# Kernel optimization log

Hardware: AMD Instinct MI355X
Metric: run time of the kernel (lower is better)

The kernel has to match this reference:

```python
import jax, jax.numpy as jnp
import numpy as np

H = 128          # hidden_channels
N_USER = 500000
N_ANIME = 20000
N_EDGE = 500000


def setup_inputs() -> dict:
    key = jax.random.key(0)
    k = jax.random.split(key, 8)
    s1 = 1.0 / np.sqrt(2 * H)   # torch Linear init scale (uniform bound)
    s2 = 1.0 / np.sqrt(H)
    return {
        "z_user": jax.random.normal(k[0], (N_USER, H), dtype=jnp.float32),
        "z_anime": jax.random.normal(k[1], (N_ANIME, H), dtype=jnp.float32),
        "row": jax.random.randint(k[2], (N_EDGE,), 0, N_USER, dtype=jnp.int64 if jax.config.jax_enable_x64 else jnp.int32),
        "col": jax.random.randint(k[3], (N_EDGE,), 0, N_ANIME, dtype=jnp.int64 if jax.config.jax_enable_x64 else jnp.int32),
        "W1": jax.random.uniform(k[4], (2 * H, H), minval=-s1, maxval=s1, dtype=jnp.float32),
        "b1": jnp.zeros((H,), dtype=jnp.float32),
        "W2": jax.random.uniform(k[5], (H, 1), minval=-s2, maxval=s2, dtype=jnp.float32),
        "b2": jnp.zeros((1,), dtype=jnp.float32),
    }


def reference(z_user, z_anime, row, col, W1, b1, W2, b2):
    zu = z_user[row]            # [E, H] gather
    za = z_anime[col]           # [E, H] gather
    # cat([zu, za], -1) @ W1 == zu @ W1[:H] + za @ W1[H:]  (avoids materializing concat)
    h = zu @ W1[:H] + za @ W1[H:] + b1          # [E, H]
    h = jax.nn.relu(h)
    out = h @ W2 + b2                            # [E, 1]
    return out.reshape(-1)
```

## Files before the change

kernel.cpp:

```cpp
#include <hip/hip_runtime.h>
#include <hip/hip_bf16.h>
#include <stdint.h>

#define H_ 128
#define THREADS 256
#define EPB 64

typedef __bf16 bf16x8 __attribute__((ext_vector_type(8)));
typedef float  f32x4  __attribute__((ext_vector_type(4)));


__device__ inline bf16x8 pack8(float4 a, float4 b) {
    bf16x8 v;
    v[0] = (__bf16)a.x; v[1] = (__bf16)a.y; v[2] = (__bf16)a.z; v[3] = (__bf16)a.w;
    v[4] = (__bf16)b.x; v[5] = (__bf16)b.y; v[6] = (__bf16)b.z; v[7] = (__bf16)b.w;
    return v;
}

__global__ void prep_kernel(const float* __restrict__ W1,
                            const float* __restrict__ za,
                            __bf16* __restrict__ wfrag,
                            __bf16* __restrict__ za_bf,
                            int nza) {
    int t = blockIdx.x * 256 + threadIdx.x;
    if (t < 32768) {
        int j  = t & 7;
        int ln = (t >> 3) & 63;
        int nt = (t >> 9) & 7;
        int ks = (t >> 12) & 7;
        int k  = ks * 32 + ((ln >> 4) << 3) + j;
        int n  = nt * 16 + (ln & 15);
        wfrag[t] = (__bf16)W1[k * H_ + n];
    } else {
        long i = (long)(t - 32768) * 8;
        if (i < nza) {
            float4 a = *(const float4*)(za + i);
            float4 b = *(const float4*)(za + i + 4);
            *(bf16x8*)(za_bf + i) = pack8(a, b);
        }
    }
}

__global__ __launch_bounds__(THREADS, 4)
void edge_decoder_kernel(const float* __restrict__ z_user,
                         const float* __restrict__ z_anime,
                         const int*   __restrict__ row,
                         const int*   __restrict__ col,
                         const float* __restrict__ W1,
                         const float* __restrict__ b1,
                         const float* __restrict__ W2,
                         const float* __restrict__ b2,
                         const __bf16* __restrict__ wfrag,
                         const __bf16* __restrict__ za_bf,
                         int use_ws,
                         float* __restrict__ out,
                         int E) {
    __shared__ bf16x8 Bf[4][8][64];

    const int tid  = threadIdx.x;
    const int lane = tid & 63;
    const int wv   = tid >> 6;
    const int g    = lane >> 4;
    const int m    = lane & 15;
    const int base = blockIdx.x * EPB + wv * 16;

    int e = base + m; if (e >= E) e = E - 1;
    const int r0 = row[e], c0 = col[e];

    float4 xu[8];
    {
        const float* zu = z_user + (size_t)r0 * H_ + g * 8;
        #pragma unroll
        for (int ks = 0; ks < 4; ++ks) {
            xu[2 * ks]     = *(const float4*)(zu + ks * 32);
            xu[2 * ks + 1] = *(const float4*)(zu + ks * 32 + 4);
        }
    }
    bf16x8 Aa[4];
    if (use_ws) {
        const __bf16* za = za_bf + (size_t)c0 * H_ + g * 8;
        #pragma unroll
        for (int ks = 0; ks < 4; ++ks)
            Aa[ks] = *(const bf16x8*)(za + ks * 32);
    }

    float w2v[8], b1v[8];
    #pragma unroll
    for (int nt = 0; nt < 8; ++nt) { int ch = nt * 16 + m; w2v[nt] = W2[ch]; b1v[nt] = b1[ch]; }
    const float bb = b2[0];

    if (use_ws) {
        const int4* src = (const int4*)wfrag;
        int4*       dst = (int4*)&Bf[0][0][0];
        #pragma unroll
        for (int i = 0; i < 8; ++i)
            dst[tid + i * THREADS] = src[tid + i * THREADS];
    } else {
        __bf16* d = (__bf16*)&Bf[0][0][0];
        for (int idx = tid; idx < H_ * H_; idx += THREADS) {
            int k = idx >> 7, n = idx & 127;
            int ks = k >> 5, gg = (k >> 3) & 3, j = k & 7;
            int nt = n >> 4, ln = (gg << 4) | (n & 15);
            d[ks * 4096 + nt * 512 + ln * 8 + j] = (__bf16)W1[k * H_ + n];
        }
    }
    __syncthreads();

    bf16x8 Au[4];
    #pragma unroll
    for (int ks = 0; ks < 4; ++ks)
        Au[ks] = pack8(xu[2 * ks], xu[2 * ks + 1]);

    f32x4 acc[8];
    #pragma unroll
    for (int nt = 0; nt < 8; ++nt) acc[nt] = (f32x4){0.f, 0.f, 0.f, 0.f};

    #pragma unroll
    for (int nt = 0; nt < 8; ++nt) {
        #pragma unroll
        for (int ks = 0; ks < 4; ++ks) {
            bf16x8 b = Bf[ks][nt][lane];
            acc[nt] = __builtin_amdgcn_mfma_f32_16x16x32_bf16(Au[ks], b, acc[nt], 0, 0, 0);
        }
    }

    if (!use_ws) {
        const float* za = z_anime + (size_t)c0 * H_ + g * 8;
        #pragma unroll
        for (int ks = 0; ks < 4; ++ks)
            Aa[ks] = pack8(*(const float4*)(za + ks * 32),
                           *(const float4*)(za + ks * 32 + 4));
    }

    __syncthreads();

    if (use_ws) {
        const int4* src = (const int4*)wfrag + 2048;
        int4*       dst = (int4*)&Bf[0][0][0];
        #pragma unroll
        for (int i = 0; i < 8; ++i)
            dst[tid + i * THREADS] = src[tid + i * THREADS];
    } else {
        __bf16* d = (__bf16*)&Bf[0][0][0];
        for (int idx = tid; idx < H_ * H_; idx += THREADS) {
            int k = idx >> 7, n = idx & 127;
            int ks = k >> 5, gg = (k >> 3) & 3, j = k & 7;
            int nt = n >> 4, ln = (gg << 4) | (n & 15);
            d[ks * 4096 + nt * 512 + ln * 8 + j] = (__bf16)W1[(H_ + k) * H_ + n];
        }
    }
    __syncthreads();

    #pragma unroll
    for (int nt = 0; nt < 8; ++nt) {
        #pragma unroll
        for (int ks = 0; ks < 4; ++ks) {
            bf16x8 b = Bf[ks][nt][lane];
            acc[nt] = __builtin_amdgcn_mfma_f32_16x16x32_bf16(Aa[ks], b, acc[nt], 0, 0, 0);
        }
    }

    float ps[4];
    #pragma unroll
    for (int r = 0; r < 4; ++r) {
        float s = 0.f;
        #pragma unroll
        for (int nt = 0; nt < 8; ++nt) {
            float h = acc[nt][r] + b1v[nt];
            s = fmaf(fmaxf(h, 0.f), w2v[nt], s);
        }
        ps[r] = s;
    }
    #pragma unroll
    for (int off = 1; off < 16; off <<= 1) {
        #pragma unroll
        for (int r = 0; r < 4; ++r)
            ps[r] += __shfl_xor(ps[r], off, 64);
    }
    if (m == 0) {
        int eb = base + g * 4;
        if (eb + 3 < E) {
            float4 o = make_float4(ps[0] + bb, ps[1] + bb, ps[2] + bb, ps[3] + bb);
            *(float4*)(out + eb) = o;
        } else {
            #pragma unroll
            for (int r = 0; r < 4; ++r)
                if (eb + r < E) out[eb + r] = ps[r] + bb;
        }
    }
}

extern "C" void kernel_launch(void* const* d_in, const int* in_sizes, int n_in,
                              void* d_out, int out_size, void* d_ws, size_t ws_size,
                              hipStream_t stream) {
    const float* z_user  = (const float*)d_in[0];
    const float* z_anime = (const float*)d_in[1];
    const int*   row     = (const int*)d_in[2];
    const int*   col     = (const int*)d_in[3];
    const float* W1      = (const float*)d_in[4];
    const float* b1      = (const float*)d_in[5];
    const float* W2      = (const float*)d_in[6];
    const float* b2      = (const float*)d_in[7];
    float*       out     = (float*)d_out;
    const int E   = in_sizes[2];
    const int nza = in_sizes[1];

    const size_t wfrag_bytes = 2u * H_ * H_ * sizeof(__bf16);
    const size_t need = wfrag_bytes + (size_t)nza * sizeof(__bf16);
    int use_ws = (d_ws != nullptr && ws_size >= need) ? 1 : 0;

    __bf16* wfrag = (__bf16*)d_ws;
    __bf16* za_bf = (__bf16*)((char*)d_ws + wfrag_bytes);

    if (use_ws) {
        int za_threads = (nza + 7) / 8;
        int nb_prep = 128 + (za_threads + 255) / 256;
        prep_kernel<<<nb_prep, 256, 0, stream>>>(W1, z_anime, wfrag, za_bf, nza);
    }

    int nb = (E + EPB - 1) / EPB;
    edge_decoder_kernel<<<nb, THREADS, 0, stream>>>(
        z_user, z_anime, row, col, W1, b1, W2, b2,
        wfrag, za_bf, use_ws, out, E);
}
```

Baseline: 78.23 us.

## Bucket-sort edges by user row and remap workgroups per XCD for locality

Adds a per-call counting sort of edges into row buckets (histogram, three-stage scan, scatter) so that consecutive workgroups gather nearby z_user rows. The decoder then reads the permuted row and col arrays and writes each result back through the permutation. Block indices are also remapped so that each XCD processes a contiguous range of sorted edges, which is meant to improve L2 reuse. The cost is five extra kernel launches, about 2 MB of extra index traffic, and scattered output stores. With roughly one edge per user row the locality gain may be small.

Measured after the change: 173.6 us. 122% more time.

```diff
diff --git a/kernel.cpp b/kernel.cpp
--- a/kernel.cpp
+++ b/kernel.cpp
@@ -5,6 +5,9 @@
 #define H_ 128
 #define THREADS 256
 #define EPB 64
+#define NBUCKET 8192
+#define NPART 16
+#define TS_SORT 1024
 
 typedef __bf16 bf16x8 __attribute__((ext_vector_type(8)));
 typedef float  f32x4  __attribute__((ext_vector_type(4)));
@@ -41,11 +44,103 @@
     }
 }
 
+__global__ __launch_bounds__(TS_SORT)
+void hist_kernel(const int* __restrict__ row, int* __restrict__ part,
+                 int E, int shift) {
+    __shared__ int h[NBUCKET];
+    const int p = blockIdx.x, tid = threadIdx.x;
+    #pragma unroll
+    for (int j = 0; j < NBUCKET / TS_SORT; ++j) h[tid + j * TS_SORT] = 0;
+    __syncthreads();
+    const int chunk = (E + NPART - 1) / NPART;
+    const int s = p * chunk, e = min(s + chunk, E);
+    for (int i = s + tid; i < e; i += TS_SORT)
+        atomicAdd(&h[row[i] >> shift], 1);
+    __syncthreads();
+    #pragma unroll
+    for (int j = 0; j < NBUCKET / TS_SORT; ++j)
+        part[p * NBUCKET + tid + j * TS_SORT] = h[tid + j * TS_SORT];
+}
+
+__global__ void scanA_kernel(const int* __restrict__ part, int* __restrict__ btot) {
+    int b = blockIdx.x * 256 + threadIdx.x;
+    int s = 0;
+    #pragma unroll 4
+    for (int p = 0; p < NPART; ++p) s += part[p * NBUCKET + b];
+    btot[b] = s;
+}
+
+__global__ __launch_bounds__(1024)
+void scanB_kernel(const int* __restrict__ btot, int* __restrict__ bbase) {
+    __shared__ int wsum[16];
+    const int t = threadIdx.x;
+    int v[8]; int s = 0;
+    #pragma unroll
+    for (int j = 0; j < 8; ++j) { v[j] = btot[t * 8 + j]; s += v[j]; }
+    const int lane = t & 63, wv = t >> 6;
+    int inc = s;
+    #pragma unroll
+    for (int off = 1; off < 64; off <<= 1) {
+        int x = __shfl_up(inc, off, 64);
+        if (lane >= off) inc += x;
+    }
+    if (lane == 63) wsum[wv] = inc;
+    __syncthreads();
+    if (wv == 0 && lane < 16) {
+        int ws = wsum[lane];
+        #pragma unroll
+        for (int off = 1; off < 16; off <<= 1) {
+            int x = __shfl_up(ws, off, 64);
+            if (lane >= off) ws += x;
+        }
+        wsum[lane] = ws;
+    }
+    __syncthreads();
+    int excl = ((wv > 0) ? wsum[wv - 1] : 0) + inc - s;
+    #pragma unroll
+    for (int j = 0; j < 8; ++j) { bbase[t * 8 + j] = excl; excl += v[j]; }
+}
+
+__global__ void scanC_kernel(int* __restrict__ part, const int* __restrict__ bbase) {
+    int b = blockIdx.x * 256 + threadIdx.x;
+    int run = bbase[b];
+    #pragma unroll 4
+    for (int p = 0; p < NPART; ++p) {
+        int idx = p * NBUCKET + b;
+        int x = part[idx];
+        part[idx] = run;
+        run += x;
+    }
+}
+
+__global__ __launch_bounds__(TS_SORT)
+void scatter_kernel(const int* __restrict__ row, const int* __restrict__ col,
+                    const int* __restrict__ part,
+                    int* __restrict__ rowp, int* __restrict__ colp,
+                    int* __restrict__ perm, int E, int shift) {
+    __shared__ int pos[NBUCKET];
+    const int p = blockIdx.x, tid = threadIdx.x;
+    #pragma unroll
+    for (int j = 0; j < NBUCKET / TS_SORT; ++j)
+        pos[tid + j * TS_SORT] = part[p * NBUCKET + tid + j * TS_SORT];
+    __syncthreads();
+    const int chunk = (E + NPART - 1) / NPART;
+    const int s = p * chunk, e = min(s + chunk, E);
+    for (int i = s + tid; i < e; i += TS_SORT) {
+        int r = row[i], c = col[i];
+        int slot = atomicAdd(&pos[r >> shift], 1);
+        rowp[slot] = r;
+        colp[slot] = c;
+        perm[slot] = i;
+    }
+}
+
 __global__ __launch_bounds__(THREADS, 4)
 void edge_decoder_kernel(const float* __restrict__ z_user,
                          const float* __restrict__ z_anime,
                          const int*   __restrict__ row,
                          const int*   __restrict__ col,
+                         const int*   __restrict__ perm,
                          const float* __restrict__ W1,
                          const float* __restrict__ b1,
                          const float* __restrict__ W2,
@@ -54,15 +149,24 @@
                          const __bf16* __restrict__ za_bf,
                          int use_ws,
                          float* __restrict__ out,
-                         int E) {
+                         int E, int nwg) {
     __shared__ bf16x8 Bf[4][8][64];
+
+    int wg = blockIdx.x;
+    if (perm) {
+        const int nx = 8;
+        int q = nwg / nx, r = nwg % nx;
+        int xcd = wg % nx, idx = wg / nx;
+        int basewg = (xcd < r) ? xcd * (q + 1) : r * (q + 1) + (xcd - r) * q;
+        wg = basewg + idx;
+    }
 
     const int tid  = threadIdx.x;
     const int lane = tid & 63;
     const int wv   = tid >> 6;
     const int g    = lane >> 4;
     const int m    = lane & 15;
-    const int base = blockIdx.x * EPB + wv * 16;
+    const int base = wg * EPB + wv * 16;
 
     int e = base + m; if (e >= E) e = E - 1;
     const int r0 = row[e], c0 = col[e];
@@ -179,7 +283,19 @@
     }
     if (m == 0) {
         int eb = base + g * 4;
-        if (eb + 3 < E) {
+        if (perm) {
+            if (eb + 3 < E) {
+                int4 p4 = *(const int4*)(perm + eb);
+                out[p4.x] = ps[0] + bb;
+                out[p4.y] = ps[1] + bb;
+                out[p4.z] = ps[2] + bb;
+                out[p4.w] = ps[3] + bb;
+            } else {
+                #pragma unroll
+                for (int r = 0; r < 4; ++r)
+                    if (eb + r < E) out[perm[eb + r]] = ps[r] + bb;
+            }
+        } else if (eb + 3 < E) {
             float4 o = make_float4(ps[0] + bb, ps[1] + bb, ps[2] + bb, ps[3] + bb);
             *(float4*)(out + eb) = o;
         } else {
@@ -204,13 +320,32 @@
     float*       out     = (float*)d_out;
     const int E   = in_sizes[2];
     const int nza = in_sizes[1];
+    const int nu  = in_sizes[0] / H_;
+
+    const int nb   = (E + EPB - 1) / EPB;
+    const int Epad = nb * EPB;
 
     const size_t wfrag_bytes = 2u * H_ * H_ * sizeof(__bf16);
-    const size_t need = wfrag_bytes + (size_t)nza * sizeof(__bf16);
-    int use_ws = (d_ws != nullptr && ws_size >= need) ? 1 : 0;
-
-    __bf16* wfrag = (__bf16*)d_ws;
-    __bf16* za_bf = (__bf16*)((char*)d_ws + wfrag_bytes);
+    const size_t za_bytes    = ((size_t)nza * sizeof(__bf16) + 255) & ~255ull;
+    const size_t part_bytes  = (size_t)NPART * NBUCKET * sizeof(int);
+    const size_t btot_bytes  = (size_t)NBUCKET * sizeof(int);
+    const size_t idx_bytes   = ((size_t)Epad * sizeof(int) + 255) & ~255ull;
+
+    const size_t need_basic = wfrag_bytes + za_bytes;
+    const size_t need_sort  = need_basic + part_bytes + 2 * btot_bytes + 3 * idx_bytes;
+
+    int use_ws   = (d_ws != nullptr && ws_size >= need_basic) ? 1 : 0;
+    int use_sort = (d_ws != nullptr && ws_size >= need_sort) ? 1 : 0;
+
+    char* p = (char*)d_ws;
+    __bf16* wfrag = (__bf16*)p;   p += wfrag_bytes;
+    __bf16* za_bf = (__bf16*)p;   p += za_bytes;
+    int*    part  = (int*)p;      p += part_bytes;
+    int*    btot  = (int*)p;      p += btot_bytes;
+    int*    bbase = (int*)p;      p += btot_bytes;
+    int*    rowp  = (int*)p;      p += idx_bytes;
+    int*    colp  = (int*)p;      p += idx_bytes;
+    int*    perm  = (int*)p;
 
     if (use_ws) {
         int za_threads = (nza + 7) / 8;
@@ -218,8 +353,23 @@
         prep_kernel<<<nb_prep, 256, 0, stream>>>(W1, z_anime, wfrag, za_bf, nza);
     }
 
-    int nb = (E + EPB - 1) / EPB;
-    edge_decoder_kernel<<<nb, THREADS, 0, stream>>>(
-        z_user, z_anime, row, col, W1, b1, W2, b2,
-        wfrag, za_bf, use_ws, out, E);
-}
+    if (use_sort) {
+        int shift = 0;
+        while ((nu >> shift) >= NBUCKET) shift++;
+
+        hist_kernel<<<NPART, TS_SORT, 0, stream>>>(row, part, E, shift);
+        scanA_kernel<<<NBUCKET / 256, 256, 0, stream>>>(part, btot);
+        scanB_kernel<<<1, 1024, 0, stream>>>(btot, bbase);
+        scanC_kernel<<<NBUCKET / 256, 256, 0, stream>>>(part, bbase);
+        scatter_kernel<<<NPART, TS_SORT, 0, stream>>>(row, col, part,
+                                                      rowp, colp, perm, E, shift);
+
+        edge_decoder_kernel<<<nb, THREADS, 0, stream>>>(
+            z_user, z_anime, rowp, colp, perm, W1, b1, W2, b2,
+            wfrag, za_bf, 1, out, E, nb);
+    } else {
+        edge_decoder_kernel<<<nb, THREADS, 0, stream>>>(
+            z_user, z_anime, row, col, nullptr, W1, b1, W2, b2,
+            wfrag, za_bf, use_ws, out, E, nb);
+    }
+}
```

## Stage full W1 in LDS once via direct global-to-LDS loads with 8 waves

Applied to the files above, without the earlier changes.

Doubles the block to 8 waves and 128 edges and enlarges the shared buffer to hold both halves of W1 (64KB). The weights are loaded once, using global_load_lds DMA instead of going through registers, which removes one barrier pair and the mid-kernel reload. The user and anime MFMAs are merged into a single loop. Per-block weight staging is amortised over twice as many edges, but occupancy drops because of the larger LDS footprint and launch bounds of 2.

Result: faster. 75.23 us (-3.8%).

```diff
diff --git a/kernel.cpp b/kernel.cpp
--- a/kernel.cpp
+++ b/kernel.cpp
@@ -3,8 +3,9 @@
 #include <stdint.h>
 
 #define H_ 128
-#define THREADS 256
-#define EPB 64
+#define NW 8
+#define THREADS (NW * 64)
+#define EPB 128
 
 typedef __bf16 bf16x8 __attribute__((ext_vector_type(8)));
 typedef float  f32x4  __attribute__((ext_vector_type(4)));
@@ -41,7 +42,11 @@
     }
 }
 
-__global__ __launch_bounds__(THREADS, 4)
+#define GLD16(gp, lp) __builtin_amdgcn_global_load_lds(                      \
+    (const __attribute__((address_space(1))) void*)(gp),                     \
+    (__attribute__((address_space(3))) void*)(lp), 16, 0, 0)
+
+__global__ __launch_bounds__(THREADS, 2)
 void edge_decoder_kernel(const float* __restrict__ z_user,
                          const float* __restrict__ z_anime,
                          const int*   __restrict__ row,
@@ -55,7 +60,7 @@
                          int use_ws,
                          float* __restrict__ out,
                          int E) {
-    __shared__ bf16x8 Bf[4][8][64];
+    __shared__ bf16x8 Bf[8][8][64];
 
     const int tid  = threadIdx.x;
     const int lane = tid & 63;
@@ -82,34 +87,36 @@
         #pragma unroll
         for (int ks = 0; ks < 4; ++ks)
             Aa[ks] = *(const bf16x8*)(za + ks * 32);
-    }
-
-    float w2v[8], b1v[8];
-    #pragma unroll
-    for (int nt = 0; nt < 8; ++nt) { int ch = nt * 16 + m; w2v[nt] = W2[ch]; b1v[nt] = b1[ch]; }
-    const float bb = b2[0];
+    } else {
+        const float* za = z_anime + (size_t)c0 * H_ + g * 8;
+        #pragma unroll
+        for (int ks = 0; ks < 4; ++ks)
+            Aa[ks] = pack8(*(const float4*)(za + ks * 32),
+                           *(const float4*)(za + ks * 32 + 4));
+    }
 
     if (use_ws) {
-        const int4* src = (const int4*)wfrag;
-        int4*       dst = (int4*)&Bf[0][0][0];
+        const char* src = (const char*)wfrag + wv * 8192 + lane * 16;
+        char*       dst = (char*)&Bf[0][0][0] + wv * 8192;
         #pragma unroll
         for (int i = 0; i < 8; ++i)
-            dst[tid + i * THREADS] = src[tid + i * THREADS];
+            GLD16(src + i * 1024, dst + i * 1024);
     } else {
         __bf16* d = (__bf16*)&Bf[0][0][0];
-        for (int idx = tid; idx < H_ * H_; idx += THREADS) {
+        for (int idx = tid; idx < 2 * H_ * H_; idx += THREADS) {
             int k = idx >> 7, n = idx & 127;
             int ks = k >> 5, gg = (k >> 3) & 3, j = k & 7;
             int nt = n >> 4, ln = (gg << 4) | (n & 15);
             d[ks * 4096 + nt * 512 + ln * 8 + j] = (__bf16)W1[k * H_ + n];
         }
     }
-    __syncthreads();
 
     bf16x8 Au[4];
     #pragma unroll
     for (int ks = 0; ks < 4; ++ks)
         Au[ks] = pack8(xu[2 * ks], xu[2 * ks + 1]);
+
+    __syncthreads();
 
     f32x4 acc[8];
     #pragma unroll
@@ -122,43 +129,17 @@
             bf16x8 b = Bf[ks][nt][lane];
             acc[nt] = __builtin_amdgcn_mfma_f32_16x16x32_bf16(Au[ks], b, acc[nt], 0, 0, 0);
         }
-    }
-
-    if (!use_ws) {
-        const float* za = z_anime + (size_t)c0 * H_ + g * 8;
-        #pragma unroll
-        for (int ks = 0; ks < 4; ++ks)
-            Aa[ks] = pack8(*(const float4*)(za + ks * 32),
-                           *(const float4*)(za + ks * 32 + 4));
-    }
-
-    __syncthreads();
-
-    if (use_ws) {
-        const int4* src = (const int4*)wfrag + 2048;
-        int4*       dst = (int4*)&Bf[0][0][0];
-        #pragma unroll
-        for (int i = 0; i < 8; ++i)
-            dst[tid + i * THREADS] = src[tid + i * THREADS];
-    } else {
-        __bf16* d = (__bf16*)&Bf[0][0][0];
-        for (int idx = tid; idx < H_ * H_; idx += THREADS) {
-            int k = idx >> 7, n = idx & 127;
-            int ks = k >> 5, gg = (k >> 3) & 3, j = k & 7;
-            int nt = n >> 4, ln = (gg << 4) | (n & 15);
-            d[ks * 4096 + nt * 512 + ln * 8 + j] = (__bf16)W1[(H_ + k) * H_ + n];
-        }
-    }
-    __syncthreads();
-
-    #pragma unroll
-    for (int nt = 0; nt < 8; ++nt) {
         #pragma unroll
         for (int ks = 0; ks < 4; ++ks) {
-            bf16x8 b = Bf[ks][nt][lane];
+            bf16x8 b = Bf[4 + ks][nt][lane];
             acc[nt] = __builtin_amdgcn_mfma_f32_16x16x32_bf16(Aa[ks], b, acc[nt], 0, 0, 0);
         }
     }
+
+    float w2v[8], b1v[8];
+    #pragma unroll
+    for (int nt = 0; nt < 8; ++nt) { int ch = nt * 16 + m; w2v[nt] = W2[ch]; b1v[nt] = b1[ch]; }
+    const float bb = b2[0];
 
     float ps[4];
     #pragma unroll
```
